# Kernel optimization log

Measured on AMD Instinct MI355X. Metric: run time of the kernel, lower is better.

Reference implementation:

```python
import jax, jax.numpy as jnp
import numpy as np

HIDDEN_DIM = 2048
CODE_DIM = 256
CODEBOOK_SIZE = 512
FC_DIMS = [1024, 512]
BATCH = 16384
EPS = 1e-5
NEG_SLOPE = 0.01  # PyTorch LeakyReLU default


def _linear_init(key, fan_in, fan_out):
    # kaiming_uniform_(a=sqrt(3)) ~= U(-1/sqrt(fan_in), 1/sqrt(fan_in)) scaled; use uniform bound
    bound = 1.0 / np.sqrt(fan_in)
    return jax.random.uniform(key, (fan_in, fan_out), jnp.float32, -bound, bound)


def setup_inputs() -> dict:
    key = jax.random.key(0)
    ks = jax.random.split(key, 16)
    h = jax.random.normal(ks[0], (BATCH, HIDDEN_DIM), jnp.float32)
    # encoder: Linear(2048->1024, no bias), BN, LReLU, Linear(1024->512, no bias), BN, LReLU, Linear(512->256, bias)
    enc_w1 = _linear_init(ks[1], HIDDEN_DIM, FC_DIMS[0])
    enc_bn1_g = jnp.ones((FC_DIMS[0],), jnp.float32)
    enc_bn1_b = jnp.zeros((FC_DIMS[0],), jnp.float32)
    enc_w2 = _linear_init(ks[2], FC_DIMS[0], FC_DIMS[1])
    enc_bn2_g = jnp.ones((FC_DIMS[1],), jnp.float32)
    enc_bn2_b = jnp.zeros((FC_DIMS[1],), jnp.float32)
    enc_w3 = _linear_init(ks[3], FC_DIMS[1], CODE_DIM)
    enc_b3 = jax.random.uniform(ks[4], (CODE_DIM,), jnp.float32, -1/np.sqrt(FC_DIMS[1]), 1/np.sqrt(FC_DIMS[1]))
    # codebook: NearestEmbed weight shape (code_dim, codebook_size)
    codebook = jax.random.normal(ks[5], (CODE_DIM, CODEBOOK_SIZE), jnp.float32)
    # decoder: Linear(256->512, no bias), BN, LReLU, Linear(512->1024, no bias), BN, LReLU, Linear(1024->2048, bias)
    dec_w1 = _linear_init(ks[6], CODE_DIM, FC_DIMS[1])
    dec_bn1_g = jnp.ones((FC_DIMS[1],), jnp.float32)
    dec_bn1_b = jnp.zeros((FC_DIMS[1],), jnp.float32)
    dec_w2 = _linear_init(ks[7], FC_DIMS[1], FC_DIMS[0])
    dec_bn2_g = jnp.ones((FC_DIMS[0],), jnp.float32)
    dec_bn2_b = jnp.zeros((FC_DIMS[0],), jnp.float32)
    dec_w3 = _linear_init(ks[8], FC_DIMS[0], HIDDEN_DIM)
    dec_b3 = jax.random.uniform(ks[9], (HIDDEN_DIM,), jnp.float32, -1/np.sqrt(FC_DIMS[0]), 1/np.sqrt(FC_DIMS[0]))
    return dict(h=h, enc_w1=enc_w1, enc_bn1_g=enc_bn1_g, enc_bn1_b=enc_bn1_b,
                enc_w2=enc_w2, enc_bn2_g=enc_bn2_g, enc_bn2_b=enc_bn2_b,
                enc_w3=enc_w3, enc_b3=enc_b3, codebook=codebook,
                dec_w1=dec_w1, dec_bn1_g=dec_bn1_g, dec_bn1_b=dec_bn1_b,
                dec_w2=dec_w2, dec_bn2_g=dec_bn2_g, dec_bn2_b=dec_bn2_b,
                dec_w3=dec_w3, dec_b3=dec_b3)


def _bn(x, g, b):
    # BatchNorm1d, training mode: biased batch variance, eps=1e-5
    mu = jnp.mean(x, axis=0)
    var = jnp.var(x, axis=0)
    return (x - mu) * jax.lax.rsqrt(var + EPS) * g + b


def _lrelu(x):
    return jnp.where(x >= 0, x, NEG_SLOPE * x)


def _quantize(z_e, codebook):
    # nearest codebook entry; codebook is [code_dim, K]
    # dist[b,k] = ||z_e[b] - codebook[:,k]||^2 (expanded, drop constant ||z||^2 for argmin? keep full for clarity)
    d = (jnp.sum(z_e * z_e, axis=1, keepdims=True)
         - 2.0 * (z_e @ codebook)
         + jnp.sum(codebook * codebook, axis=0)[None, :])  # [B, K]
    idx = jnp.argmin(d, axis=1)  # [B]
    z_q = codebook.T[idx]        # [B, code_dim]
    return z_q, idx


def reference(h, enc_w1, enc_bn1_g, enc_bn1_b, enc_w2, enc_bn2_g, enc_bn2_b,
              enc_w3, enc_b3, codebook,
              dec_w1, dec_bn1_g, dec_bn1_b, dec_w2, dec_bn2_g, dec_bn2_b,
              dec_w3, dec_b3):
    # encoder
    x = _lrelu(_bn(h @ enc_w1, enc_bn1_g, enc_bn1_b))
    x = _lrelu(_bn(x @ enc_w2, enc_bn2_g, enc_bn2_b))
    z_e = x @ enc_w3 + enc_b3  # [B, code_dim]
    # nearest-embed quantization with straight-through estimator
    z_q_raw, code_indices = _quantize(z_e, codebook)
    z_q = z_e + jax.lax.stop_gradient(z_q_raw - z_e)
    # decoder
    y = _lrelu(_bn(z_q @ dec_w1, dec_bn1_g, dec_bn1_b))
    y = _lrelu(_bn(y @ dec_w2, dec_bn2_g, dec_bn2_b))
    h_recon = y @ dec_w3 + dec_b3  # [B, hidden_dim]
    return z_e, z_q, h_recon, code_indices
```

## Files before the change

kernel.cpp:

```cpp
#include <hip/hip_runtime.h>
#include <hip/hip_fp16.h>
#include <cstdint>
#include <cstddef>

typedef _Float16 f16;
typedef _Float16 half8 __attribute__((ext_vector_type(8)));
typedef _Float16 half4 __attribute__((ext_vector_type(4)));
typedef float floatx4 __attribute__((ext_vector_type(4)));

static constexpr size_t NB  = 16384;
static constexpr size_t DH  = 2048;
static constexpr size_t F1  = 1024;
static constexpr size_t F2  = 512;
static constexpr size_t CD  = 256;
static constexpr size_t KCB = 512;

static constexpr size_t ZE_OFF  = 0;
static constexpr size_t ZQ_OFF  = NB * CD;
static constexpr size_t HR_OFF  = 2 * NB * CD;
static constexpr size_t IDX_OFF = 2 * NB * CD + NB * DH;

static constexpr size_t O_HH   = 0;
static constexpr size_t O_HL   = O_HH + NB * DH * 2;
static constexpr size_t R1_END = O_HL + NB * DH * 2;

static constexpr size_t R_X1H = 0;
static constexpr size_t R_X1L = NB * F1 * 2;
static constexpr size_t R_X2F = 2 * NB * F1 * 2;
static constexpr size_t R_X2H = R_X2F + NB * F2 * 4;
static constexpr size_t R_X2L = R_X2H + NB * F2 * 2;
static constexpr size_t R_Y1F = 0;
static constexpr size_t R_Y1H = NB * F2 * 4;
static constexpr size_t R_Y2H = 0;

static constexpr size_t O_W1H = R1_END;
static constexpr size_t O_W1L = O_W1H + F1 * DH * 2;
static constexpr size_t O_W2H = O_W1L + F1 * DH * 2;
static constexpr size_t O_W2L = O_W2H + F2 * F1 * 2;
static constexpr size_t O_W3H = O_W2L + F2 * F1 * 2;
static constexpr size_t O_W3L = O_W3H + CD * F2 * 2;
static constexpr size_t O_CBH = O_W3L + CD * F2 * 2;
static constexpr size_t O_CBL = O_CBH + KCB * CD * 2;
static constexpr size_t O_DW1 = O_CBL + KCB * CD * 2;
static constexpr size_t O_DW2 = O_DW1 + F2 * CD * 2;
static constexpr size_t O_DW3 = O_DW2 + F1 * F2 * 2;
static constexpr size_t O_SUM = O_DW3 + DH * F1 * 2;
static constexpr size_t O_SQ  = O_SUM + 4 * 1024 * 8;
static constexpr size_t O_SC  = O_SQ + 4 * 1024 * 8;
static constexpr size_t O_SH  = O_SC + 4 * 1024 * 4;
static constexpr size_t O_CN  = O_SH + 4 * 1024 * 4;
static constexpr size_t R2    = (O_CN + 4096 + 255) & ~(size_t)255;
static constexpr size_t R2_X1F = R2;
static constexpr size_t R2_ZEH = R2;
static constexpr size_t R2_ZEL = R2 + NB * CD * 2;
static constexpr size_t R2_S   = R2 + 2 * NB * CD * 2;
static constexpr size_t R2_ZQH = R2_S + NB * KCB * 4;
static constexpr size_t R2_Y2F = R2;

#define GLLDS(src, dst)                                                          \
    __builtin_amdgcn_global_load_lds(                                            \
        (const __attribute__((address_space(1))) void*)(src),                    \
        (__attribute__((address_space(3))) void*)(dst), 16, 0, 0)

#define VMCNT(n)  asm volatile("s_waitcnt vmcnt(" #n ")" ::: "memory")
#define LGKMCNT0  asm volatile("s_waitcnt lgkmcnt(0)" ::: "memory")

template<bool BIAS, bool STATS>
__global__ __launch_bounds__(512)
void gemm3_8ph(const f16* __restrict__ Ah_, const f16* __restrict__ Al_,
               const f16* __restrict__ Bh_, const f16* __restrict__ Bl_,
               float* __restrict__ C, const float* __restrict__ bias,
               double* __restrict__ ssum, double* __restrict__ ssq,
               int M, int N, int K)
{
    __shared__ f16 lds[2][2][16384];
    const int tid  = threadIdx.x;
    const int lane = tid & 63;
    const int w    = tid >> 6;
    const int wr   = w >> 2, wn = w & 3;
    const int row0 = blockIdx.x * 256;
    const int col0 = blockIdx.y * 256;

    const int rr8 = lane >> 3;
    const int p   = (lane & 7) ^ rr8;
    const int rr  = w * 32 + rr8;
    const f16* srcH = (p < 4) ? (Ah_ + (size_t)(row0 + rr) * K + p * 8)
                              : (Bh_ + (size_t)(col0 + rr) * K + (p - 4) * 8);
    const f16* srcL = (p < 4) ? (Al_ + (size_t)(row0 + rr) * K + p * 8)
                              : (Bl_ + (size_t)(col0 + rr) * K + (p - 4) * 8);
    const int dstBase = w * 32 * 64;
    const int KT = K >> 5;

    floatx4 acc[8][4];
#pragma unroll
    for (int m = 0; m < 8; ++m)
#pragma unroll
        for (int n = 0; n < 4; ++n)
#pragma unroll
            for (int j = 0; j < 4; ++j) acc[m][n][j] = 0.f;

    const int l15 = lane & 15;
    const int sA  = lane >> 4;

#pragma unroll
    for (int j = 0; j < 4; ++j)
        GLLDS(srcH + (size_t)j * 8 * K, &lds[0][0][dstBase + j * 512]);
#pragma unroll
    for (int j = 0; j < 4; ++j)
        GLLDS(srcL + (size_t)j * 8 * K, &lds[0][1][dstBase + j * 512]);
    VMCNT(4);
    __builtin_amdgcn_s_barrier();

    half8 afh[8], afl[8], bfh[4], bfl[4];

    for (int kt = 0; kt < KT; ++kt) {
        const int cur = kt & 1, nxt = cur ^ 1;
        const int koff = (kt + 1 < KT ? kt + 1 : kt) << 5;
        const f16* plH = lds[cur][0];
        const f16* plL = lds[cur][1];

#pragma unroll
        for (int m = 0; m < 8; ++m) {
            const int rA = wr * 128 + m * 16 + l15;
            afh[m] = *(const half8*)(plH + rA * 64 + (((sA) ^ (rA & 7)) << 3));
        }
#pragma unroll
        for (int n = 0; n < 4; ++n) {
            const int rB = wn * 64 + n * 16 + l15;
            bfh[n] = *(const half8*)(plH + rB * 64 + (((4 + sA) ^ (rB & 7)) << 3));
        }
#pragma unroll
        for (int j = 0; j < 4; ++j)
            GLLDS(srcH + (size_t)j * 8 * K + koff, &lds[nxt][0][dstBase + j * 512]);
        VMCNT(4);
        __builtin_amdgcn_s_barrier();
        LGKMCNT0;
        __builtin_amdgcn_sched_barrier(0);
        __builtin_amdgcn_s_setprio(1);
#pragma unroll
        for (int m = 0; m < 8; ++m)
#pragma unroll
            for (int n = 0; n < 4; ++n)
                acc[m][n] = __builtin_amdgcn_mfma_f32_16x16x32_f16(afh[m], bfh[n], acc[m][n], 0, 0, 0);
        __builtin_amdgcn_s_setprio(0);
        __builtin_amdgcn_s_barrier();

#pragma unroll
        for (int n = 0; n < 4; ++n) {
            const int rB = wn * 64 + n * 16 + l15;
            bfl[n] = *(const half8*)(plL + rB * 64 + (((4 + sA) ^ (rB & 7)) << 3));
        }
#pragma unroll
        for (int j = 0; j < 2; ++j)
            GLLDS(srcL + (size_t)j * 8 * K + koff, &lds[nxt][1][dstBase + j * 512]);
        __builtin_amdgcn_s_barrier();
        LGKMCNT0;
        __builtin_amdgcn_sched_barrier(0);
        __builtin_amdgcn_s_setprio(1);
#pragma unroll
        for (int m = 0; m < 8; ++m)
#pragma unroll
            for (int n = 0; n < 4; ++n)
                acc[m][n] = __builtin_amdgcn_mfma_f32_16x16x32_f16(afh[m], bfl[n], acc[m][n], 0, 0, 0);
        __builtin_amdgcn_s_setprio(0);
        __builtin_amdgcn_s_barrier();

#pragma unroll
        for (int m = 0; m < 8; ++m) {
            const int rA = wr * 128 + m * 16 + l15;
            afl[m] = *(const half8*)(plL + rA * 64 + (((sA) ^ (rA & 7)) << 3));
        }
#pragma unroll
        for (int j = 2; j < 4; ++j)
            GLLDS(srcL + (size_t)j * 8 * K + koff, &lds[nxt][1][dstBase + j * 512]);
        VMCNT(4);
        __builtin_amdgcn_s_barrier();
        LGKMCNT0;
        __builtin_amdgcn_sched_barrier(0);
        __builtin_amdgcn_s_setprio(1);
#pragma unroll
        for (int m = 0; m < 8; ++m)
#pragma unroll
            for (int n = 0; n < 4; ++n)
                acc[m][n] = __builtin_amdgcn_mfma_f32_16x16x32_f16(afl[m], bfh[n], acc[m][n], 0, 0, 0);
        __builtin_amdgcn_s_setprio(0);
        __builtin_amdgcn_s_barrier();
    }
    VMCNT(0);

    const int cb0 = col0 + wn * 64;
    const int rb0 = row0 + wr * 128 + (lane >> 4) * 4;
#pragma unroll
    for (int n = 0; n < 4; ++n) {
        const int col = cb0 + n * 16 + l15;
        const float bv = BIAS ? bias[col] : 0.f;
        double sd = 0.0, sq = 0.0;
#pragma unroll
        for (int m = 0; m < 8; ++m) {
            const int row = rb0 + m * 16;
#pragma unroll
            for (int j = 0; j < 4; ++j) {
                const float v = acc[m][n][j] + bv;
                C[(size_t)(row + j) * N + col] = v;
                if (STATS) { sd += (double)v; sq += (double)v * (double)v; }
            }
        }
        if (STATS) {
            sd += __shfl_xor(sd, 16);
            sd += __shfl_xor(sd, 32);
            sq += __shfl_xor(sq, 16);
            sq += __shfl_xor(sq, 32);
            if (lane < 16) {
                atomicAdd(ssum + col, sd);
                atomicAdd(ssq + col, sq);
            }
        }
    }
}

template<bool BIAS, bool STATS>
__global__ __launch_bounds__(512)
void gemm1_8ph(const f16* __restrict__ A_, const f16* __restrict__ B_,
               float* __restrict__ C, const float* __restrict__ bias,
               double* __restrict__ ssum, double* __restrict__ ssq,
               int M, int N, int K)
{
    __shared__ f16 lds[3][16384];
    const int tid  = threadIdx.x;
    const int lane = tid & 63;
    const int w    = tid >> 6;
    const int wr   = w >> 2, wn = w & 3;
    const int row0 = blockIdx.x * 256;
    const int col0 = blockIdx.y * 256;

    const int rr8 = lane >> 3;
    const int p   = (lane & 7) ^ rr8;
    const int rr  = w * 32 + rr8;
    const f16* srcH = (p < 4) ? (A_ + (size_t)(row0 + rr) * K + p * 8)
                              : (B_ + (size_t)(col0 + rr) * K + (p - 4) * 8);
    const int dstBase = w * 32 * 64;
    const int KT = K >> 5;

    floatx4 acc[8][4];
#pragma unroll
    for (int m = 0; m < 8; ++m)
#pragma unroll
        for (int n = 0; n < 4; ++n)
#pragma unroll
            for (int j = 0; j < 4; ++j) acc[m][n][j] = 0.f;

    const int l15 = lane & 15;
    const int sA  = lane >> 4;

#pragma unroll
    for (int j = 0; j < 4; ++j)
        GLLDS(srcH + (size_t)j * 8 * K, &lds[0][dstBase + j * 512]);
    {
        const int k1 = (KT > 1 ? 1 : 0) << 5;
#pragma unroll
        for (int j = 0; j < 4; ++j)
            GLLDS(srcH + (size_t)j * 8 * K + k1, &lds[1][dstBase + j * 512]);
    }
    VMCNT(4);
    __builtin_amdgcn_s_barrier();

    half8 afh[8], bfh[4];

    for (int kt = 0; kt < KT; ++kt) {
        const int cur = kt % 3, tgt = (kt + 2) % 3;
        const int koff = (kt + 2 < KT ? kt + 2 : KT - 1) << 5;
        const f16* plH = lds[cur];

#pragma unroll
        for (int m = 0; m < 8; ++m) {
            const int rA = wr * 128 + m * 16 + l15;
            afh[m] = *(const half8*)(plH + rA * 64 + (((sA) ^ (rA & 7)) << 3));
        }
#pragma unroll
        for (int n = 0; n < 4; ++n) {
            const int rB = wn * 64 + n * 16 + l15;
            bfh[n] = *(const half8*)(plH + rB * 64 + (((4 + sA) ^ (rB & 7)) << 3));
        }
#pragma unroll
        for (int j = 0; j < 2; ++j)
            GLLDS(srcH + (size_t)j * 8 * K + koff, &lds[tgt][dstBase + j * 512]);
        __builtin_amdgcn_s_barrier();
        LGKMCNT0;
        __builtin_amdgcn_sched_barrier(0);
        __builtin_amdgcn_s_setprio(1);
#pragma unroll
        for (int m = 0; m < 8; ++m)
#pragma unroll
            for (int n = 0; n < 2; ++n)
                acc[m][n] = __builtin_amdgcn_mfma_f32_16x16x32_f16(afh[m], bfh[n], acc[m][n], 0, 0, 0);
        __builtin_amdgcn_s_setprio(0);
        __builtin_amdgcn_s_barrier();

#pragma unroll
        for (int j = 2; j < 4; ++j)
            GLLDS(srcH + (size_t)j * 8 * K + koff, &lds[tgt][dstBase + j * 512]);
        VMCNT(4);
        __builtin_amdgcn_s_barrier();
        __builtin_amdgcn_s_setprio(1);
#pragma unroll
        for (int m = 0; m < 8; ++m)
#pragma unroll
            for (int n = 2; n < 4; ++n)
                acc[m][n] = __builtin_amdgcn_mfma_f32_16x16x32_f16(afh[m], bfh[n], acc[m][n], 0, 0, 0);
        __builtin_amdgcn_s_setprio(0);
        __builtin_amdgcn_s_barrier();
    }
    VMCNT(0);

    const int cb0 = col0 + wn * 64;
    const int rb0 = row0 + wr * 128 + (lane >> 4) * 4;
#pragma unroll
    for (int n = 0; n < 4; ++n) {
        const int col = cb0 + n * 16 + l15;
        const float bv = BIAS ? bias[col] : 0.f;
        double sd = 0.0, sq = 0.0;
#pragma unroll
        for (int m = 0; m < 8; ++m) {
            const int row = rb0 + m * 16;
#pragma unroll
            for (int j = 0; j < 4; ++j) {
                const float v = acc[m][n][j] + bv;
                C[(size_t)(row + j) * N + col] = v;
                if (STATS) { sd += (double)v; sq += (double)v * (double)v; }
            }
        }
        if (STATS) {
            sd += __shfl_xor(sd, 16);
            sd += __shfl_xor(sd, 32);
            sq += __shfl_xor(sq, 16);
            sq += __shfl_xor(sq, 32);
            if (lane < 16) {
                atomicAdd(ssum + col, sd);
                atomicAdd(ssq + col, sq);
            }
        }
    }
}

__global__ void split_f32(const float* __restrict__ X, f16* __restrict__ hi,
                          f16* __restrict__ lo, size_t n4)
{
    const size_t stride = (size_t)gridDim.x * blockDim.x;
    for (size_t i = (size_t)blockIdx.x * blockDim.x + threadIdx.x; i < n4; i += stride) {
        const floatx4 x = ((const floatx4*)X)[i];
        half4 h, l;
#pragma unroll
        for (int j = 0; j < 4; ++j) {
            const float v = x[j];
            const f16 hv = (f16)v;
            h[j] = hv;
            l[j] = (f16)(v - (float)hv);
        }
        ((half4*)hi)[i] = h;
        ((half4*)lo)[i] = l;
    }
}

template<bool SPLIT>
__global__ void bn_apply(const float* __restrict__ X, const float* __restrict__ scale,
                         const float* __restrict__ shift, f16* __restrict__ Yhi,
                         f16* __restrict__ Ylo, size_t n4, int Nmask)
{
    const size_t stride = (size_t)gridDim.x * blockDim.x;
    for (size_t i = (size_t)blockIdx.x * blockDim.x + threadIdx.x; i < n4; i += stride) {
        const floatx4 x = ((const floatx4*)X)[i];
        const int col = (int)((i * 4) & (size_t)Nmask);
        half4 h, l;
#pragma unroll
        for (int j = 0; j < 4; ++j) {
            float v = x[j] * scale[col + j] + shift[col + j];
            v = v >= 0.f ? v : 0.01f * v;
            const f16 hv = (f16)v;
            h[j] = hv;
            if (SPLIT) l[j] = (f16)(v - (float)hv);
        }
        ((half4*)Yhi)[i] = h;
        if (SPLIT) ((half4*)Ylo)[i] = l;
    }
}

__global__ void bn_finalize(const double* __restrict__ ssum, const double* __restrict__ ssq,
                            const float* __restrict__ g, const float* __restrict__ b,
                            float* __restrict__ scale, float* __restrict__ shift, int N)
{
    const int j = blockIdx.x * blockDim.x + threadIdx.x;
    if (j < N) {
        const double inv = 1.0 / (double)NB;
        const double mean = ssum[j] * inv;
        const double var  = ssq[j] * inv - mean * mean;
        const double sc   = (double)g[j] / sqrt(var + 1e-5);
        scale[j] = (float)sc;
        shift[j] = (float)((double)b[j] - mean * sc);
    }
}

template<bool SPLIT>
__global__ void transpose_split(const float* __restrict__ W, f16* __restrict__ Thi,
                                f16* __restrict__ Tlo, int K, int N)
{
    __shared__ float tile[32][33];
    const int x = threadIdx.x;
    const int y = threadIdx.y;
    const int nt = blockIdx.x * 32;
    const int kt = blockIdx.y * 32;
#pragma unroll
    for (int i = 0; i < 32; i += 8)
        tile[y + i][x] = W[(size_t)(kt + y + i) * N + nt + x];
    __syncthreads();
#pragma unroll
    for (int i = 0; i < 32; i += 8) {
        const float v = tile[x][y + i];
        const size_t o = (size_t)(nt + y + i) * K + kt + x;
        const f16 hv = (f16)v;
        Thi[o] = hv;
        if (SPLIT) Tlo[o] = (f16)(v - (float)hv);
    }
}

__global__ void cnorm_kernel(const float* __restrict__ cb, float* __restrict__ cn)
{
    const int k = blockIdx.x * blockDim.x + threadIdx.x;
    if (k < (int)KCB) {
        double s = 0.0;
        for (int d = 0; d < (int)CD; ++d) {
            const float v = cb[(size_t)d * KCB + k];
            s += (double)v * v;
        }
        cn[k] = (float)s;
    }
}

__global__ void argmin_gather(const float* __restrict__ S, const float* __restrict__ cn,
                              const float* __restrict__ cb, float* __restrict__ zq,
                              float* __restrict__ idx_out, f16* __restrict__ zqh)
{
    const int lane = threadIdx.x & 63;
    const int row  = blockIdx.x * 4 + (threadIdx.x >> 6);
    const float* Sr = S + (size_t)row * KCB;
    float best = 3.4e38f;
    int bi = 0;
#pragma unroll
    for (int i = 0; i < 8; ++i) {
        const int k = lane + 64 * i;
        const float d = cn[k] - 2.f * Sr[k];
        if (d < best) { best = d; bi = k; }
    }
#pragma unroll
    for (int off = 32; off > 0; off >>= 1) {
        const float ob = __shfl_xor(best, off);
        const int   oi = __shfl_xor(bi, off);
        if (ob < best || (ob == best && oi < bi)) { best = ob; bi = oi; }
    }
    if (lane == 0) idx_out[row] = (float)bi;
#pragma unroll
    for (int i = 0; i < 4; ++i) {
        const int d = lane + 64 * i;
        const float v = cb[(size_t)d * KCB + bi];
        zq[(size_t)row * CD + d]  = v;
        zqh[(size_t)row * CD + d] = (f16)v;
    }
}

extern "C" void kernel_launch(void* const* d_in, const int* in_sizes, int n_in,
                              void* d_out, int out_size, void* d_ws, size_t ws_size,
                              hipStream_t stream)
{
    (void)in_sizes; (void)n_in; (void)out_size; (void)ws_size;
    const float* h   = (const float*)d_in[0];
    const float* ew1 = (const float*)d_in[1];
    const float* bg1 = (const float*)d_in[2];
    const float* bb1 = (const float*)d_in[3];
    const float* ew2 = (const float*)d_in[4];
    const float* bg2 = (const float*)d_in[5];
    const float* bb2 = (const float*)d_in[6];
    const float* ew3 = (const float*)d_in[7];
    const float* eb3 = (const float*)d_in[8];
    const float* cb  = (const float*)d_in[9];
    const float* dw1 = (const float*)d_in[10];
    const float* dg1 = (const float*)d_in[11];
    const float* db1 = (const float*)d_in[12];
    const float* dw2 = (const float*)d_in[13];
    const float* dg2 = (const float*)d_in[14];
    const float* db2 = (const float*)d_in[15];
    const float* dw3 = (const float*)d_in[16];
    const float* db3 = (const float*)d_in[17];

    char* ws = (char*)d_ws;
    float* out = (float*)d_out;

    f16* Hh  = (f16*)(ws + O_HH);
    f16* Hl  = (f16*)(ws + O_HL);
    f16* W1h = (f16*)(ws + O_W1H);
    f16* W1l = (f16*)(ws + O_W1L);
    f16* W2h = (f16*)(ws + O_W2H);
    f16* W2l = (f16*)(ws + O_W2L);
    f16* W3h = (f16*)(ws + O_W3H);
    f16* W3l = (f16*)(ws + O_W3L);
    f16* CBh = (f16*)(ws + O_CBH);
    f16* CBl = (f16*)(ws + O_CBL);
    f16* D1t = (f16*)(ws + O_DW1);
    f16* D2t = (f16*)(ws + O_DW2);
    f16* D3t = (f16*)(ws + O_DW3);
    double* sum0 = (double*)(ws + O_SUM);
    double* sq0  = (double*)(ws + O_SQ);
    float* sc0 = (float*)(ws + O_SC);
    float* sh0 = (float*)(ws + O_SH);
    float* cn  = (float*)(ws + O_CN);

    float* X1f = (float*)(ws + R2_X1F);
    f16*  X1h = (f16*)(ws + R_X1H);
    f16*  X1l = (f16*)(ws + R_X1L);
    float* X2f = (float*)(ws + R_X2F);
    f16*  X2h = (f16*)(ws + R_X2H);
    f16*  X2l = (f16*)(ws + R_X2L);
    f16*  Zeh = (f16*)(ws + R2_ZEH);
    f16*  Zel = (f16*)(ws + R2_ZEL);
    float* Sb  = (float*)(ws + R2_S);
    f16*  Zqh = (f16*)(ws + R2_ZQH);
    float* Y1f = (float*)(ws + R_Y1F);
    f16*  Y1h = (f16*)(ws + R_Y1H);
    float* Y2f = (float*)(ws + R2_Y2F);
    f16*  Y2h = (f16*)(ws + R_Y2H);

    hipMemsetAsync(ws + O_SUM, 0, 4 * 1024 * 8 * 2, stream);

    split_f32<<<2048, 256, 0, stream>>>(h, Hh, Hl, NB * DH / 4);
    transpose_split<true ><<<dim3(F1 / 32, DH / 32), dim3(32, 8), 0, stream>>>(ew1, W1h, W1l, DH, F1);
    transpose_split<true ><<<dim3(F2 / 32, F1 / 32), dim3(32, 8), 0, stream>>>(ew2, W2h, W2l, F1, F2);
    transpose_split<true ><<<dim3(CD / 32, F2 / 32), dim3(32, 8), 0, stream>>>(ew3, W3h, W3l, F2, CD);
    transpose_split<true ><<<dim3(KCB / 32, CD / 32), dim3(32, 8), 0, stream>>>(cb, CBh, CBl, CD, KCB);
    transpose_split<false><<<dim3(F2 / 32, CD / 32), dim3(32, 8), 0, stream>>>(dw1, D1t, nullptr, CD, F2);
    transpose_split<false><<<dim3(F1 / 32, F2 / 32), dim3(32, 8), 0, stream>>>(dw2, D2t, nullptr, F2, F1);
    transpose_split<false><<<dim3(DH / 32, F1 / 32), dim3(32, 8), 0, stream>>>(dw3, D3t, nullptr, F1, DH);

    gemm3_8ph<false, true><<<dim3(NB / 256, F1 / 256), 512, 0, stream>>>(
        Hh, Hl, W1h, W1l, X1f, nullptr, sum0, sq0, NB, F1, DH);
    bn_finalize<<<4, 256, 0, stream>>>(sum0, sq0, bg1, bb1, sc0, sh0, F1);
    bn_apply<true><<<2048, 256, 0, stream>>>(X1f, sc0, sh0, X1h, X1l, NB * F1 / 4, (int)F1 - 1);

    gemm3_8ph<false, true><<<dim3(NB / 256, F2 / 256), 512, 0, stream>>>(
        X1h, X1l, W2h, W2l, X2f, nullptr, sum0 + 1024, sq0 + 1024, NB, F2, F1);
    bn_finalize<<<2, 256, 0, stream>>>(sum0 + 1024, sq0 + 1024, bg2, bb2, sc0 + 1024, sh0 + 1024, F2);
    bn_apply<true><<<2048, 256, 0, stream>>>(X2f, sc0 + 1024, sh0 + 1024, X2h, X2l, NB * F2 / 4, (int)F2 - 1);

    gemm3_8ph<true, false><<<dim3(NB / 256, CD / 256), 512, 0, stream>>>(
        X2h, X2l, W3h, W3l, out + ZE_OFF, eb3, nullptr, nullptr, NB, CD, F2);

    split_f32<<<2048, 256, 0, stream>>>(out + ZE_OFF, Zeh, Zel, NB * CD / 4);
    cnorm_kernel<<<2, 256, 0, stream>>>(cb, cn);
    gemm3_8ph<false, false><<<dim3(NB / 256, KCB / 256), 512, 0, stream>>>(
        Zeh, Zel, CBh, CBl, Sb, nullptr, nullptr, nullptr, NB, KCB, CD);
    argmin_gather<<<NB / 4, 256, 0, stream>>>(Sb, cn, cb, out + ZQ_OFF, out + IDX_OFF, Zqh);

    gemm1_8ph<false, true><<<dim3(NB / 256, F2 / 256), 512, 0, stream>>>(
        Zqh, D1t, Y1f, nullptr, sum0 + 2048, sq0 + 2048, NB, F2, CD);
    bn_finalize<<<2, 256, 0, stream>>>(sum0 + 2048, sq0 + 2048, dg1, db1, sc0 + 2048, sh0 + 2048, F2);
    bn_apply<false><<<2048, 256, 0, stream>>>(Y1f, sc0 + 2048, sh0 + 2048, Y1h, nullptr, NB * F2 / 4, (int)F2 - 1);

    gemm1_8ph<false, true><<<dim3(NB / 256, F1 / 256), 512, 0, stream>>>(
        Y1h, D2t, Y2f, nullptr, sum0 + 3072, sq0 + 3072, NB, F1, F2);
    bn_finalize<<<4, 256, 0, stream>>>(sum0 + 3072, sq0 + 3072, dg2, db2, sc0 + 3072, sh0 + 3072, F1);
    bn_apply<false><<<2048, 256, 0, stream>>>(Y2f, sc0 + 3072, sh0 + 3072, Y2h, nullptr, NB * F1 / 4, (int)F1 - 1);

    gemm1_8ph<true, false><<<dim3(NB / 256, DH / 256), 512, 0, stream>>>(
        Y2h, D3t, out + HR_OFF, db3, nullptr, nullptr, NB, DH, F1);
}
```

Measured before the change: 633.4 us.

## Fuse BN-apply, LeakyReLU and fp16 split into GEMM A-operand loads

```diff
diff --git a/kernel.cpp b/kernel.cpp
--- a/kernel.cpp
+++ b/kernel.cpp
@@ -1,11 +1,9 @@
 #include <hip/hip_runtime.h>
-#include <hip/hip_fp16.h>
 #include <cstdint>
 #include <cstddef>
 
 typedef _Float16 f16;
 typedef _Float16 half8 __attribute__((ext_vector_type(8)));
-typedef _Float16 half4 __attribute__((ext_vector_type(4)));
 typedef float floatx4 __attribute__((ext_vector_type(4)));
 
 static constexpr size_t NB  = 16384;
@@ -20,20 +18,7 @@
 static constexpr size_t HR_OFF  = 2 * NB * CD;
 static constexpr size_t IDX_OFF = 2 * NB * CD + NB * DH;
 
-static constexpr size_t O_HH   = 0;
-static constexpr size_t O_HL   = O_HH + NB * DH * 2;
-static constexpr size_t R1_END = O_HL + NB * DH * 2;
-
-static constexpr size_t R_X1H = 0;
-static constexpr size_t R_X1L = NB * F1 * 2;
-static constexpr size_t R_X2F = 2 * NB * F1 * 2;
-static constexpr size_t R_X2H = R_X2F + NB * F2 * 4;
-static constexpr size_t R_X2L = R_X2H + NB * F2 * 2;
-static constexpr size_t R_Y1F = 0;
-static constexpr size_t R_Y1H = NB * F2 * 4;
-static constexpr size_t R_Y2H = 0;
-
-static constexpr size_t O_W1H = R1_END;
+static constexpr size_t O_W1H = 0;
 static constexpr size_t O_W1L = O_W1H + F1 * DH * 2;
 static constexpr size_t O_W2H = O_W1L + F1 * DH * 2;
 static constexpr size_t O_W2L = O_W2H + F2 * F1 * 2;
@@ -49,13 +34,9 @@
 static constexpr size_t O_SC  = O_SQ + 4 * 1024 * 8;
 static constexpr size_t O_SH  = O_SC + 4 * 1024 * 4;
 static constexpr size_t O_CN  = O_SH + 4 * 1024 * 4;
-static constexpr size_t R2    = (O_CN + 4096 + 255) & ~(size_t)255;
-static constexpr size_t R2_X1F = R2;
-static constexpr size_t R2_ZEH = R2;
-static constexpr size_t R2_ZEL = R2 + NB * CD * 2;
-static constexpr size_t R2_S   = R2 + 2 * NB * CD * 2;
-static constexpr size_t R2_ZQH = R2_S + NB * KCB * 4;
-static constexpr size_t R2_Y2F = R2;
+static constexpr size_t O_X1F = (O_CN + 4096 + 255) & ~(size_t)255;
+static constexpr size_t O_X2F = O_X1F + NB * F1 * 4;
+static constexpr size_t O_SB  = O_X2F + NB * F2 * 4;
 
 #define GLLDS(src, dst)                                                          \
     __builtin_amdgcn_global_load_lds(                                            \
@@ -65,32 +46,51 @@
 #define VMCNT(n)  asm volatile("s_waitcnt vmcnt(" #n ")" ::: "memory")
 #define LGKMCNT0  asm volatile("s_waitcnt lgkmcnt(0)" ::: "memory")
 
-template<bool BIAS, bool STATS>
+template<bool AFF, bool BIAS, bool STATS>
 __global__ __launch_bounds__(512)
-void gemm3_8ph(const f16* __restrict__ Ah_, const f16* __restrict__ Al_,
-               const f16* __restrict__ Bh_, const f16* __restrict__ Bl_,
-               float* __restrict__ C, const float* __restrict__ bias,
-               double* __restrict__ ssum, double* __restrict__ ssq,
-               int M, int N, int K)
-{
-    __shared__ f16 lds[2][2][16384];
-    const int tid  = threadIdx.x;
-    const int lane = tid & 63;
-    const int w    = tid >> 6;
-    const int wr   = w >> 2, wn = w & 3;
-    const int row0 = blockIdx.x * 256;
-    const int col0 = blockIdx.y * 256;
-
-    const int rr8 = lane >> 3;
-    const int p   = (lane & 7) ^ rr8;
-    const int rr  = w * 32 + rr8;
-    const f16* srcH = (p < 4) ? (Ah_ + (size_t)(row0 + rr) * K + p * 8)
-                              : (Bh_ + (size_t)(col0 + rr) * K + (p - 4) * 8);
-    const f16* srcL = (p < 4) ? (Al_ + (size_t)(row0 + rr) * K + p * 8)
-                              : (Bl_ + (size_t)(col0 + rr) * K + (p - 4) * 8);
-    const int dstBase = w * 32 * 64;
+void gemm3f(const float* __restrict__ Af, const f16* __restrict__ Bh_,
+            const f16* __restrict__ Bl_, const float* __restrict__ scale,
+            const float* __restrict__ shift, float* __restrict__ C,
+            const float* __restrict__ bias, double* __restrict__ ssum,
+            double* __restrict__ ssq, int M, int N, int K)
+{
+    __shared__ f16 sA[2][16384];
+    __shared__ f16 sBH[2][8192];
+    __shared__ f16 sBL[2][8192];
+    const int tid = threadIdx.x, lane = tid & 63, w = tid >> 6;
+    const int wr = w >> 2, wn = w & 3;
+    const int row0 = blockIdx.x * 256, col0 = blockIdx.y * 256;
     const int KT = K >> 5;
 
+    const int ar = lane >> 2, aks = lane & 3;
+    const int rwA0 = w * 32 + ar, rwA1 = rwA0 + 16;
+    const size_t offA0 = (size_t)(row0 + rwA0) * K + aks * 8;
+    const size_t offA1 = (size_t)(row0 + rwA1) * K + aks * 8;
+    const int wH0 = rwA0 * 64 + ((aks ^ (rwA0 & 7)) << 3);
+    const int wL0 = rwA0 * 64 + (((aks + 4) ^ (rwA0 & 7)) << 3);
+    const int wH1 = rwA1 * 64 + ((aks ^ (rwA1 & 7)) << 3);
+    const int wL1 = rwA1 * 64 + (((aks + 4) ^ (rwA1 & 7)) << 3);
+
+    const int rr8 = lane >> 3, sp = lane & 7, p = sp ^ rr8;
+    const size_t offB0 = (size_t)(col0 + 2 * (w * 16 + 0 + rr8) + (p >> 2)) * K + (p & 3) * 8;
+    const size_t offB1 = (size_t)(col0 + 2 * (w * 16 + 8 + rr8) + (p >> 2)) * K + (p & 3) * 8;
+    const int dB0 = (w * 16 + 0) * 64, dB1 = (w * 16 + 8) * 64;
+
+    const int l15 = lane & 15, sl = lane >> 4;
+    int rdAH[8], rdAL[8], rdB[4];
+#pragma unroll
+    for (int m = 0; m < 8; ++m) {
+        const int rA = wr * 128 + m * 16 + l15;
+        rdAH[m] = rA * 64 + ((sl ^ (rA & 7)) << 3);
+        rdAL[m] = rA * 64 + (((4 + sl) ^ (rA & 7)) << 3);
+    }
+#pragma unroll
+    for (int n = 0; n < 4; ++n) {
+        const int rB = wn * 64 + n * 16 + l15;
+        const int q = rB >> 1;
+        rdB[n] = q * 64 + (((((rB & 1) << 2) + sl) ^ (q & 7)) << 3);
+    }
+
     floatx4 acc[8][4];
 #pragma unroll
     for (int m = 0; m < 8; ++m)
@@ -99,16 +99,43 @@
 #pragma unroll
             for (int j = 0; j < 4; ++j) acc[m][n][j] = 0.f;
 
-    const int l15 = lane & 15;
-    const int sA  = lane >> 4;
-
-#pragma unroll
-    for (int j = 0; j < 4; ++j)
-        GLLDS(srcH + (size_t)j * 8 * K, &lds[0][0][dstBase + j * 512]);
-#pragma unroll
-    for (int j = 0; j < 4; ++j)
-        GLLDS(srcL + (size_t)j * 8 * K, &lds[0][1][dstBase + j * 512]);
+    floatx4 u0a, u0b, u1a, u1b, sv0, sv1, hv0, hv1;
+
+    auto cvt_write = [&](int dst) {
+        half8 hh, ll;
+#pragma unroll
+        for (int j = 0; j < 4; ++j) {
+            float v = u0a[j];
+            if constexpr (AFF) { v = fmaf(v, sv0[j], hv0[j]); v = v >= 0.f ? v : 0.01f * v; }
+            f16 t = (f16)v; hh[j] = t; ll[j] = (f16)(v - (float)t);
+            float v2 = u0b[j];
+            if constexpr (AFF) { v2 = fmaf(v2, sv1[j], hv1[j]); v2 = v2 >= 0.f ? v2 : 0.01f * v2; }
+            f16 t2 = (f16)v2; hh[4 + j] = t2; ll[4 + j] = (f16)(v2 - (float)t2);
+        }
+        *(half8*)&sA[dst][wH0] = hh; *(half8*)&sA[dst][wL0] = ll;
+#pragma unroll
+        for (int j = 0; j < 4; ++j) {
+            float v = u1a[j];
+            if constexpr (AFF) { v = fmaf(v, sv0[j], hv0[j]); v = v >= 0.f ? v : 0.01f * v; }
+            f16 t = (f16)v; hh[j] = t; ll[j] = (f16)(v - (float)t);
+            float v2 = u1b[j];
+            if constexpr (AFF) { v2 = fmaf(v2, sv1[j], hv1[j]); v2 = v2 >= 0.f ? v2 : 0.01f * v2; }
+            f16 t2 = (f16)v2; hh[4 + j] = t2; ll[4 + j] = (f16)(v2 - (float)t2);
+        }
+        *(half8*)&sA[dst][wH1] = hh; *(half8*)&sA[dst][wL1] = ll;
+    };
+
+    u0a = *(const floatx4*)(Af + offA0);     u0b = *(const floatx4*)(Af + offA0 + 4);
+    u1a = *(const floatx4*)(Af + offA1);     u1b = *(const floatx4*)(Af + offA1 + 4);
+    if constexpr (AFF) {
+        sv0 = *(const floatx4*)(scale + aks * 8);     sv1 = *(const floatx4*)(scale + aks * 8 + 4);
+        hv0 = *(const floatx4*)(shift + aks * 8);     hv1 = *(const floatx4*)(shift + aks * 8 + 4);
+    }
+    GLLDS(Bh_ + offB0, &sBH[0][dB0]); GLLDS(Bh_ + offB1, &sBH[0][dB1]);
+    GLLDS(Bl_ + offB0, &sBL[0][dB0]); GLLDS(Bl_ + offB1, &sBL[0][dB1]);
     VMCNT(4);
+    cvt_write(0);
+    VMCNT(0); LGKMCNT0;
     __builtin_amdgcn_s_barrier();
 
     half8 afh[8], afl[8], bfh[4], bfl[4];
@@ -116,26 +143,22 @@
     for (int kt = 0; kt < KT; ++kt) {
         const int cur = kt & 1, nxt = cur ^ 1;
         const int koff = (kt + 1 < KT ? kt + 1 : kt) << 5;
-        const f16* plH = lds[cur][0];
-        const f16* plL = lds[cur][1];
-
-#pragma unroll
-        for (int m = 0; m < 8; ++m) {
-            const int rA = wr * 128 + m * 16 + l15;
-            afh[m] = *(const half8*)(plH + rA * 64 + (((sA) ^ (rA & 7)) << 3));
-        }
-#pragma unroll
-        for (int n = 0; n < 4; ++n) {
-            const int rB = wn * 64 + n * 16 + l15;
-            bfh[n] = *(const half8*)(plH + rB * 64 + (((4 + sA) ^ (rB & 7)) << 3));
-        }
-#pragma unroll
-        for (int j = 0; j < 4; ++j)
-            GLLDS(srcH + (size_t)j * 8 * K + koff, &lds[nxt][0][dstBase + j * 512]);
-        VMCNT(4);
-        __builtin_amdgcn_s_barrier();
-        LGKMCNT0;
-        __builtin_amdgcn_sched_barrier(0);
+        const f16* pA = sA[cur]; const f16* pBH = sBH[cur]; const f16* pBL = sBL[cur];
+
+#pragma unroll
+        for (int m = 0; m < 8; ++m) afh[m] = *(const half8*)(pA + rdAH[m]);
+#pragma unroll
+        for (int n = 0; n < 4; ++n) bfh[n] = *(const half8*)(pBH + rdB[n]);
+        u0a = *(const floatx4*)(Af + offA0 + koff); u0b = *(const floatx4*)(Af + offA0 + koff + 4);
+        u1a = *(const floatx4*)(Af + offA1 + koff); u1b = *(const floatx4*)(Af + offA1 + koff + 4);
+        if constexpr (AFF) {
+            sv0 = *(const floatx4*)(scale + koff + aks * 8); sv1 = *(const floatx4*)(scale + koff + aks * 8 + 4);
+            hv0 = *(const floatx4*)(shift + koff + aks * 8); hv1 = *(const floatx4*)(shift + koff + aks * 8 + 4);
+        }
+        GLLDS(Bh_ + offB0 + koff, &sBH[nxt][dB0]); GLLDS(Bh_ + offB1 + koff, &sBH[nxt][dB1]);
+        if constexpr (AFF) { VMCNT(10); } else { VMCNT(6); }
+        __builtin_amdgcn_s_barrier();
+        LGKMCNT0; __builtin_amdgcn_sched_barrier(0);
         __builtin_amdgcn_s_setprio(1);
 #pragma unroll
         for (int m = 0; m < 8; ++m)
@@ -145,17 +168,13 @@
         __builtin_amdgcn_s_setprio(0);
         __builtin_amdgcn_s_barrier();
 
-#pragma unroll
-        for (int n = 0; n < 4; ++n) {
-            const int rB = wn * 64 + n * 16 + l15;
-            bfl[n] = *(const half8*)(plL + rB * 64 + (((4 + sA) ^ (rB & 7)) << 3));
-        }
-#pragma unroll
-        for (int j = 0; j < 2; ++j)
-            GLLDS(srcL + (size_t)j * 8 * K + koff, &lds[nxt][1][dstBase + j * 512]);
-        __builtin_amdgcn_s_barrier();
-        LGKMCNT0;
-        __builtin_amdgcn_sched_barrier(0);
+        VMCNT(2);
+#pragma unroll
+        for (int n = 0; n < 4; ++n) bfl[n] = *(const half8*)(pBL + rdB[n]);
+        cvt_write(nxt);
+        GLLDS(Bl_ + offB0 + koff, &sBL[nxt][dB0]); GLLDS(Bl_ + offB1 + koff, &sBL[nxt][dB1]);
+        __builtin_amdgcn_s_barrier();
+        LGKMCNT0; __builtin_amdgcn_sched_barrier(0);
         __builtin_amdgcn_s_setprio(1);
 #pragma unroll
         for (int m = 0; m < 8; ++m)
@@ -166,17 +185,10 @@
         __builtin_amdgcn_s_barrier();
 
 #pragma unroll
-        for (int m = 0; m < 8; ++m) {
-            const int rA = wr * 128 + m * 16 + l15;
-            afl[m] = *(const half8*)(plL + rA * 64 + (((sA) ^ (rA & 7)) << 3));
-        }
-#pragma unroll
-        for (int j = 2; j < 4; ++j)
-            GLLDS(srcL + (size_t)j * 8 * K + koff, &lds[nxt][1][dstBase + j * 512]);
-        VMCNT(4);
-        __builtin_amdgcn_s_barrier();
-        LGKMCNT0;
-        __builtin_amdgcn_sched_barrier(0);
+        for (int m = 0; m < 8; ++m) afl[m] = *(const half8*)(pA + rdAL[m]);
+        VMCNT(2);
+        __builtin_amdgcn_s_barrier();
+        LGKMCNT0; __builtin_amdgcn_sched_barrier(0);
         __builtin_amdgcn_s_setprio(1);
 #pragma unroll
         for (int m = 0; m < 8; ++m)
@@ -206,41 +218,57 @@
             }
         }
         if (STATS) {
-            sd += __shfl_xor(sd, 16);
-            sd += __shfl_xor(sd, 32);
-            sq += __shfl_xor(sq, 16);
-            sq += __shfl_xor(sq, 32);
-            if (lane < 16) {
-                atomicAdd(ssum + col, sd);
-                atomicAdd(ssq + col, sq);
-            }
-        }
-    }
-}
-
-template<bool BIAS, bool STATS>
+            sd += __shfl_xor(sd, 16); sd += __shfl_xor(sd, 32);
+            sq += __shfl_xor(sq, 16); sq += __shfl_xor(sq, 32);
+            if (lane < 16) { atomicAdd(ssum + col, sd); atomicAdd(ssq + col, sq); }
+        }
+    }
+}
+
+template<bool AFF, bool BIAS, bool STATS>
 __global__ __launch_bounds__(512)
-void gemm1_8ph(const f16* __restrict__ A_, const f16* __restrict__ B_,
-               float* __restrict__ C, const float* __restrict__ bias,
-               double* __restrict__ ssum, double* __restrict__ ssq,
-               int M, int N, int K)
-{
-    __shared__ f16 lds[3][16384];
-    const int tid  = threadIdx.x;
-    const int lane = tid & 63;
-    const int w    = tid >> 6;
-    const int wr   = w >> 2, wn = w & 3;
-    const int row0 = blockIdx.x * 256;
-    const int col0 = blockIdx.y * 256;
-
-    const int rr8 = lane >> 3;
-    const int p   = (lane & 7) ^ rr8;
-    const int rr  = w * 32 + rr8;
-    const f16* srcH = (p < 4) ? (A_ + (size_t)(row0 + rr) * K + p * 8)
-                              : (B_ + (size_t)(col0 + rr) * K + (p - 4) * 8);
-    const int dstBase = w * 32 * 64;
+void gemm1f(const float* __restrict__ Af, const f16* __restrict__ Bh_,
+            const float* __restrict__ scale, const float* __restrict__ shift,
+            float* __restrict__ C, const float* __restrict__ bias,
+            double* __restrict__ ssum, double* __restrict__ ssq,
+            int M, int N, int K)
+{
+    __shared__ f16 sA[3][8192];
+    __shared__ f16 sB[3][8192];
+    const int tid = threadIdx.x, lane = tid & 63, w = tid >> 6;
+    const int wr = w >> 2, wn = w & 3;
+    const int row0 = blockIdx.x * 256, col0 = blockIdx.y * 256;
     const int KT = K >> 5;
 
+    const int aq = lane >> 3, alsl = lane & 7;
+    const int pq0 = w * 16 + aq, pq1 = pq0 + 8;
+    const int mr0 = 2 * pq0 + (alsl >> 2), mr1 = 2 * pq1 + (alsl >> 2);
+    const size_t offA0 = (size_t)(row0 + mr0) * K + (alsl & 3) * 8;
+    const size_t offA1 = (size_t)(row0 + mr1) * K + (alsl & 3) * 8;
+    const int wA0 = pq0 * 64 + ((alsl ^ (pq0 & 7)) << 3);
+    const int wA1 = pq1 * 64 + ((alsl ^ (pq1 & 7)) << 3);
+    const int aks = alsl & 3;
+
+    const int rr8 = lane >> 3, sp = lane & 7, p = sp ^ rr8;
+    const size_t offB0 = (size_t)(col0 + 2 * (w * 16 + 0 + rr8) + (p >> 2)) * K + (p & 3) * 8;
+    const size_t offB1 = (size_t)(col0 + 2 * (w * 16 + 8 + rr8) + (p >> 2)) * K + (p & 3) * 8;
+    const int dB0 = (w * 16 + 0) * 64, dB1 = (w * 16 + 8) * 64;
+
+    const int l15 = lane & 15, sl = lane >> 4;
+    int rdA[8], rdB[4];
+#pragma unroll
+    for (int m = 0; m < 8; ++m) {
+        const int rA = wr * 128 + m * 16 + l15;
+        const int q = rA >> 1;
+        rdA[m] = q * 64 + (((((rA & 1) << 2) + sl) ^ (q & 7)) << 3);
+    }
+#pragma unroll
+    for (int n = 0; n < 4; ++n) {
+        const int rB = wn * 64 + n * 16 + l15;
+        const int q = rB >> 1;
+        rdB[n] = q * 64 + (((((rB & 1) << 2) + sl) ^ (q & 7)) << 3);
+    }
+
     floatx4 acc[8][4];
 #pragma unroll
     for (int m = 0; m < 8; ++m)
@@ -249,44 +277,85 @@
 #pragma unroll
             for (int j = 0; j < 4; ++j) acc[m][n][j] = 0.f;
 
-    const int l15 = lane & 15;
-    const int sA  = lane >> 4;
-
-#pragma unroll
-    for (int j = 0; j < 4; ++j)
-        GLLDS(srcH + (size_t)j * 8 * K, &lds[0][dstBase + j * 512]);
+    floatx4 u0a, u0b, u1a, u1b, sv0, sv1, hv0, hv1;
+
+    auto cvt_write = [&](int dst) {
+        half8 hh;
+#pragma unroll
+        for (int j = 0; j < 4; ++j) {
+            float v = u0a[j];
+            if constexpr (AFF) { v = fmaf(v, sv0[j], hv0[j]); v = v >= 0.f ? v : 0.01f * v; }
+            hh[j] = (f16)v;
+            float v2 = u0b[j];
+            if constexpr (AFF) { v2 = fmaf(v2, sv1[j], hv1[j]); v2 = v2 >= 0.f ? v2 : 0.01f * v2; }
+            hh[4 + j] = (f16)v2;
+        }
+        *(half8*)&sA[dst][wA0] = hh;
+#pragma unroll
+        for (int j = 0; j < 4; ++j) {
+            float v = u1a[j];
+            if constexpr (AFF) { v = fmaf(v, sv0[j], hv0[j]); v = v >= 0.f ? v : 0.01f * v; }
+            hh[j] = (f16)v;
+            float v2 = u1b[j];
+            if constexpr (AFF) { v2 = fmaf(v2, sv1[j], hv1[j]); v2 = v2 >= 0.f ? v2 : 0.01f * v2; }
+            hh[4 + j] = (f16)v2;
+        }
+        *(half8*)&sA[dst][wA1] = hh;
+    };
+
+    floatx4 q0a = *(const floatx4*)(Af + offA0), q0b = *(const floatx4*)(Af + offA0 + 4);
+    floatx4 q1a = *(const floatx4*)(Af + offA1), q1b = *(const floatx4*)(Af + offA1 + 4);
+    floatx4 ps0, ps1, ph0, ph1;
+    if constexpr (AFF) {
+        ps0 = *(const floatx4*)(scale + aks * 8); ps1 = *(const floatx4*)(scale + aks * 8 + 4);
+        ph0 = *(const floatx4*)(shift + aks * 8); ph1 = *(const floatx4*)(shift + aks * 8 + 4);
+    }
+    GLLDS(Bh_ + offB0, &sB[0][dB0]); GLLDS(Bh_ + offB1, &sB[0][dB1]);
     {
         const int k1 = (KT > 1 ? 1 : 0) << 5;
-#pragma unroll
-        for (int j = 0; j < 4; ++j)
-            GLLDS(srcH + (size_t)j * 8 * K + k1, &lds[1][dstBase + j * 512]);
-    }
-    VMCNT(4);
+        u0a = *(const floatx4*)(Af + offA0 + k1); u0b = *(const floatx4*)(Af + offA0 + k1 + 4);
+        u1a = *(const floatx4*)(Af + offA1 + k1); u1b = *(const floatx4*)(Af + offA1 + k1 + 4);
+        if constexpr (AFF) {
+            sv0 = *(const floatx4*)(scale + k1 + aks * 8); sv1 = *(const floatx4*)(scale + k1 + aks * 8 + 4);
+            hv0 = *(const floatx4*)(shift + k1 + aks * 8); hv1 = *(const floatx4*)(shift + k1 + aks * 8 + 4);
+        }
+        GLLDS(Bh_ + offB0 + k1, &sB[1][dB0]); GLLDS(Bh_ + offB1 + k1, &sB[1][dB1]);
+    }
+    if constexpr (AFF) { VMCNT(12); } else { VMCNT(8); }
+    {
+        floatx4 t0 = u0a, t1 = u0b, t2 = u1a, t3 = u1b, s0 = sv0, s1 = sv1, h0 = hv0, h1 = hv1;
+        u0a = q0a; u0b = q0b; u1a = q1a; u1b = q1b;
+        if constexpr (AFF) { sv0 = ps0; sv1 = ps1; hv0 = ph0; hv1 = ph1; }
+        cvt_write(0);
+        u0a = t0; u0b = t1; u1a = t2; u1b = t3;
+        if constexpr (AFF) { sv0 = s0; sv1 = s1; hv0 = h0; hv1 = h1; }
+    }
+    VMCNT(2);
+    cvt_write(1);
+    LGKMCNT0;
     __builtin_amdgcn_s_barrier();
 
     half8 afh[8], bfh[4];
 
     for (int kt = 0; kt < KT; ++kt) {
-        const int cur = kt % 3, tgt = (kt + 2) % 3;
+        const int cur = kt % 3, nx2 = (kt + 2) % 3;
         const int koff = (kt + 2 < KT ? kt + 2 : KT - 1) << 5;
-        const f16* plH = lds[cur];
-
-#pragma unroll
-        for (int m = 0; m < 8; ++m) {
-            const int rA = wr * 128 + m * 16 + l15;
-            afh[m] = *(const half8*)(plH + rA * 64 + (((sA) ^ (rA & 7)) << 3));
-        }
-#pragma unroll
-        for (int n = 0; n < 4; ++n) {
-            const int rB = wn * 64 + n * 16 + l15;
-            bfh[n] = *(const half8*)(plH + rB * 64 + (((4 + sA) ^ (rB & 7)) << 3));
-        }
-#pragma unroll
-        for (int j = 0; j < 2; ++j)
-            GLLDS(srcH + (size_t)j * 8 * K + koff, &lds[tgt][dstBase + j * 512]);
-        __builtin_amdgcn_s_barrier();
-        LGKMCNT0;
-        __builtin_amdgcn_sched_barrier(0);
+        const f16* pA = sA[cur]; const f16* pB = sB[cur];
+
+#pragma unroll
+        for (int m = 0; m < 8; ++m) afh[m] = *(const half8*)(pA + rdA[m]);
+#pragma unroll
+        for (int n = 0; n < 4; ++n) bfh[n] = *(const half8*)(pB + rdB[n]);
+        u0a = *(const floatx4*)(Af + offA0 + koff); u0b = *(const floatx4*)(Af + offA0 + koff + 4);
+        u1a = *(const floatx4*)(Af + offA1 + koff); u1b = *(const floatx4*)(Af + offA1 + koff + 4);
+        if constexpr (AFF) {
+            sv0 = *(const floatx4*)(scale + koff + aks * 8); sv1 = *(const floatx4*)(scale + koff + aks * 8 + 4);
+            hv0 = *(const floatx4*)(shift + koff + aks * 8); hv1 = *(const floatx4*)(shift + koff + aks * 8 + 4);
+        }
+        GLLDS(Bh_ + offB0 + koff, &sB[nx2][dB0]); GLLDS(Bh_ + offB1 + koff, &sB[nx2][dB1]);
+        if constexpr (AFF) { VMCNT(10); } else { VMCNT(6); }
+        __builtin_amdgcn_s_barrier();
+        LGKMCNT0; __builtin_amdgcn_sched_barrier(0);
         __builtin_amdgcn_s_setprio(1);
 #pragma unroll
         for (int m = 0; m < 8; ++m)
@@ -296,11 +365,8 @@
         __builtin_amdgcn_s_setprio(0);
         __builtin_amdgcn_s_barrier();
 
-#pragma unroll
-        for (int j = 2; j < 4; ++j)
-            GLLDS(srcH + (size_t)j * 8 * K + koff, &lds[tgt][dstBase + j * 512]);
-        VMCNT(4);
-        __builtin_amdgcn_s_barrier();
+        VMCNT(2);
+        cvt_write(nx2);
         __builtin_amdgcn_s_setprio(1);
 #pragma unroll
         for (int m = 0; m < 8; ++m)
@@ -308,6 +374,7 @@
             for (int n = 2; n < 4; ++n)
                 acc[m][n] = __builtin_amdgcn_mfma_f32_16x16x32_f16(afh[m], bfh[n], acc[m][n], 0, 0, 0);
         __builtin_amdgcn_s_setprio(0);
+        LGKMCNT0;
         __builtin_amdgcn_s_barrier();
     }
     VMCNT(0);
@@ -330,57 +397,10 @@
             }
         }
         if (STATS) {
-            sd += __shfl_xor(sd, 16);
-            sd += __shfl_xor(sd, 32);
-            sq += __shfl_xor(sq, 16);
-            sq += __shfl_xor(sq, 32);
-            if (lane < 16) {
-                atomicAdd(ssum + col, sd);
-                atomicAdd(ssq + col, sq);
-            }
-        }
-    }
-}
-
-__global__ void split_f32(const float* __restrict__ X, f16* __restrict__ hi,
-                          f16* __restrict__ lo, size_t n4)
-{
-    const size_t stride = (size_t)gridDim.x * blockDim.x;
-    for (size_t i = (size_t)blockIdx.x * blockDim.x + threadIdx.x; i < n4; i += stride) {
-        const floatx4 x = ((const floatx4*)X)[i];
-        half4 h, l;
-#pragma unroll
-        for (int j = 0; j < 4; ++j) {
-            const float v = x[j];
-            const f16 hv = (f16)v;
-            h[j] = hv;
-            l[j] = (f16)(v - (float)hv);
-        }
-        ((half4*)hi)[i] = h;
-        ((half4*)lo)[i] = l;
-    }
-}
-
-template<bool SPLIT>
-__global__ void bn_apply(const float* __restrict__ X, const float* __restrict__ scale,
-                         const float* __restrict__ shift, f16* __restrict__ Yhi,
-                         f16* __restrict__ Ylo, size_t n4, int Nmask)
-{
-    const size_t stride = (size_t)gridDim.x * blockDim.x;
-    for (size_t i = (size_t)blockIdx.x * blockDim.x + threadIdx.x; i < n4; i += stride) {
-        const floatx4 x = ((const floatx4*)X)[i];
-        const int col = (int)((i * 4) & (size_t)Nmask);
-        half4 h, l;
-#pragma unroll
-        for (int j = 0; j < 4; ++j) {
-            float v = x[j] * scale[col + j] + shift[col + j];
-            v = v >= 0.f ? v : 0.01f * v;
-            const f16 hv = (f16)v;
-            h[j] = hv;
-            if (SPLIT) l[j] = (f16)(v - (float)hv);
-        }
-        ((half4*)Yhi)[i] = h;
-        if (SPLIT) ((half4*)Ylo)[i] = l;
+            sd += __shfl_xor(sd, 16); sd += __shfl_xor(sd, 32);
+            sq += __shfl_xor(sq, 16); sq += __shfl_xor(sq, 32);
+            if (lane < 16) { atomicAdd(ssum + col, sd); atomicAdd(ssq + col, sq); }
+        }
     }
 }
 
@@ -437,7 +457,7 @@
 
 __global__ void argmin_gather(const float* __restrict__ S, const float* __restrict__ cn,
                               const float* __restrict__ cb, float* __restrict__ zq,
-                              float* __restrict__ idx_out, f16* __restrict__ zqh)
+                              float* __restrict__ idx_out)
 {
     const int lane = threadIdx.x & 63;
     const int row  = blockIdx.x * 4 + (threadIdx.x >> 6);
@@ -460,9 +480,7 @@
 #pragma unroll
     for (int i = 0; i < 4; ++i) {
         const int d = lane + 64 * i;
-        const float v = cb[(size_t)d * KCB + bi];
-        zq[(size_t)row * CD + d]  = v;
-        zqh[(size_t)row * CD + d] = (f16)v;
+        zq[(size_t)row * CD + d] = cb[(size_t)d * KCB + bi];
     }
 }
 
@@ -493,8 +511,6 @@
     char* ws = (char*)d_ws;
     float* out = (float*)d_out;
 
-    f16* Hh  = (f16*)(ws + O_HH);
-    f16* Hl  = (f16*)(ws + O_HL);
     f16* W1h = (f16*)(ws + O_W1H);
     f16* W1l = (f16*)(ws + O_W1L);
     f16* W2h = (f16*)(ws + O_W2H);
@@ -511,25 +527,14 @@
     float* sc0 = (float*)(ws + O_SC);
     float* sh0 = (float*)(ws + O_SH);
     float* cn  = (float*)(ws + O_CN);
-
-    float* X1f = (float*)(ws + R2_X1F);
-    f16*  X1h = (f16*)(ws + R_X1H);
-    f16*  X1l = (f16*)(ws + R_X1L);
-    float* X2f = (float*)(ws + R_X2F);
-    f16*  X2h = (f16*)(ws + R_X2H);
-    f16*  X2l = (f16*)(ws + R_X2L);
-    f16*  Zeh = (f16*)(ws + R2_ZEH);
-    f16*  Zel = (f16*)(ws + R2_ZEL);
-    float* Sb  = (float*)(ws + R2_S);
-    f16*  Zqh = (f16*)(ws + R2_ZQH);
-    float* Y1f = (float*)(ws + R_Y1F);
-    f16*  Y1h = (f16*)(ws + R_Y1H);
-    float* Y2f = (float*)(ws + R2_Y2F);
-    f16*  Y2h = (f16*)(ws + R_Y2H);
+    float* X1f = (float*)(ws + O_X1F);
+    float* X2f = (float*)(ws + O_X2F);
+    float* Sb  = (float*)(ws + O_SB);
+    float* Y1f = X2f;
+    float* Y2f = X1f;
 
     hipMemsetAsync(ws + O_SUM, 0, 4 * 1024 * 8 * 2, stream);
 
-    split_f32<<<2048, 256, 0, stream>>>(h, Hh, Hl, NB * DH / 4);
     transpose_split<true ><<<dim3(F1 / 32, DH / 32), dim3(32, 8), 0, stream>>>(ew1, W1h, W1l, DH, F1);
     transpose_split<true ><<<dim3(F2 / 32, F1 / 32), dim3(32, 8), 0, stream>>>(ew2, W2h, W2l, F1, F2);
     transpose_split<true ><<<dim3(CD / 32, F2 / 32), dim3(32, 8), 0, stream>>>(ew3, W3h, W3l, F2, CD);
@@ -538,35 +543,30 @@
     transpose_split<false><<<dim3(F1 / 32, F2 / 32), dim3(32, 8), 0, stream>>>(dw2, D2t, nullptr, F2, F1);
     transpose_split<false><<<dim3(DH / 32, F1 / 32), dim3(32, 8), 0, stream>>>(dw3, D3t, nullptr, F1, DH);
 
-    gemm3_8ph<false, true><<<dim3(NB / 256, F1 / 256), 512, 0, stream>>>(
-        Hh, Hl, W1h, W1l, X1f, nullptr, sum0, sq0, NB, F1, DH);
+    gemm3f<false, false, true><<<dim3(NB / 256, F1 / 256), 512, 0, stream>>>(
+        h, W1h, W1l, nullptr, nullptr, X1f, nullptr, sum0, sq0, NB, F1, DH);
     bn_finalize<<<4, 256, 0, stream>>>(sum0, sq0, bg1, bb1, sc0, sh0, F1);
-    bn_apply<true><<<2048, 256, 0, stream>>>(X1f, sc0, sh0, X1h, X1l, NB * F1 / 4, (int)F1 - 1);
-
-    gemm3_8ph<false, true><<<dim3(NB / 256, F2 / 256), 512, 0, stream>>>(
-        X1h, X1l, W2h, W2l, X2f, nullptr, sum0 + 1024, sq0 + 1024, NB, F2, F1);
+
+    gemm3f<true, false, true><<<dim3(NB / 256, F2 / 256), 512, 0, stream>>>(
+        X1f, W2h, W2l, sc0, sh0, X2f, nullptr, sum0 + 1024, sq0 + 1024, NB, F2, F1);
     bn_finalize<<<2, 256, 0, stream>>>(sum0 + 1024, sq0 + 1024, bg2, bb2, sc0 + 1024, sh0 + 1024, F2);
-    bn_apply<true><<<2048, 256, 0, stream>>>(X2f, sc0 + 1024, sh0 + 1024, X2h, X2l, NB * F2 / 4, (int)F2 - 1);
-
-    gemm3_8ph<true, false><<<dim3(NB / 256, CD / 256), 512, 0, stream>>>(
-        X2h, X2l, W3h, W3l, out + ZE_OFF, eb3, nullptr, nullptr, NB, CD, F2);
-
-    split_f32<<<2048, 256, 0, stream>>>(out + ZE_OFF, Zeh, Zel, NB * CD / 4);
+
+    gemm3f<true, true, false><<<dim3(NB / 256, CD / 256), 512, 0, stream>>>(
+        X2f, W3h, W3l, sc0 + 1024, sh0 + 1024, out + ZE_OFF, eb3, nullptr, nullptr, NB, CD, F2);
+
     cnorm_kernel<<<2, 256, 0, stream>>>(cb, cn);
-    gemm3_8ph<false, false><<<dim3(NB / 256, KCB / 256), 512, 0, stream>>>(
-        Zeh, Zel, CBh, CBl, Sb, nullptr, nullptr, nullptr, NB, KCB, CD);
-    argmin_gather<<<NB / 4, 256, 0, stream>>>(Sb, cn, cb, out + ZQ_OFF, out + IDX_OFF, Zqh);
-
-    gemm1_8ph<false, true><<<dim3(NB / 256, F2 / 256), 512, 0, stream>>>(
-        Zqh, D1t, Y1f, nullptr, sum0 + 2048, sq0 + 2048, NB, F2, CD);
+    gemm3f<false, false, false><<<dim3(NB / 256, KCB / 256), 512, 0, stream>>>(
+        out + ZE_OFF, CBh, CBl, nullptr, nullptr, Sb, nullptr, nullptr, nullptr, NB, KCB, CD);
+    argmin_gather<<<NB / 4, 256, 0, stream>>>(Sb, cn, cb, out + ZQ_OFF, out + IDX_OFF);
+
+    gemm1f<false, false, true><<<dim3(NB / 256, F2 / 256), 512, 0, stream>>>(
+        out + ZQ_OFF, D1t, nullptr, nullptr, Y1f, nullptr, sum0 + 2048, sq0 + 2048, NB, F2, CD);
     bn_finalize<<<2, 256, 0, stream>>>(sum0 + 2048, sq0 + 2048, dg1, db1, sc0 + 2048, sh0 + 2048, F2);
-    bn_apply<false><<<2048, 256, 0, stream>>>(Y1f, sc0 + 2048, sh0 + 2048, Y1h, nullptr, NB * F2 / 4, (int)F2 - 1);
-
-    gemm1_8ph<false, true><<<dim3(NB / 256, F1 / 256), 512, 0, stream>>>(
-        Y1h, D2t, Y2f, nullptr, sum0 + 3072, sq0 + 3072, NB, F1, F2);
+
+    gemm1f<true, false, true><<<dim3(NB / 256, F1 / 256), 512, 0, stream>>>(
+        Y1f, D2t, sc0 + 2048, sh0 + 2048, Y2f, nullptr, sum0 + 3072, sq0 + 3072, NB, F1, F2);
     bn_finalize<<<4, 256, 0, stream>>>(sum0 + 3072, sq0 + 3072, dg2, db2, sc0 + 3072, sh0 + 3072, F1);
-    bn_apply<false><<<2048, 256, 0, stream>>>(Y2f, sc0 + 3072, sh0 + 3072, Y2h, nullptr, NB * F1 / 4, (int)F1 - 1);
-
-    gemm1_8ph<true, false><<<dim3(NB / 256, DH / 256), 512, 0, stream>>>(
-        Y2h, D3t, out + HR_OFF, db3, nullptr, nullptr, NB, DH, F1);
-}
+
+    gemm1f<true, true, false><<<dim3(NB / 256, DH / 256), 512, 0, stream>>>(
+        Y2f, D3t, sc0 + 3072, sh0 + 3072, out + HR_OFF, db3, nullptr, nullptr, NB, DH, F1);
+}
```

New measurement: 663.3 us. 4.7% more time.
